# Kernel tuning notes

Hardware: AMD Instinct MI355X
Metric: run time of the kernel (lower is better)

Reference implementation:

```python
import jax, jax.numpy as jnp
import numpy as np

N = 50000
E = 1600000
D_IN = 128
D_OUT = 128


def setup_inputs() -> dict:
    key = jax.random.key(0)
    k1, k2, k3, k4, k5 = jax.random.split(key, 5)
    feature = jax.random.normal(k1, (N, D_IN), dtype=jnp.float32)
    src = jax.random.randint(k2, (E,), 0, N, dtype=jnp.int32)
    dst = jax.random.randint(k3, (E,), 0, N, dtype=jnp.int32)
    # nn.Linear(in_feats, out_feats): weight [out, in], bias [out]
    bound = 1.0 / np.sqrt(D_IN)
    weight = jax.random.uniform(k4, (D_OUT, D_IN), minval=-bound, maxval=bound, dtype=jnp.float32)
    bias = jax.random.uniform(k5, (D_OUT,), minval=-bound, maxval=bound, dtype=jnp.float32)
    return {"feature": feature, "src": src, "dst": dst, "weight": weight, "bias": bias}


def reference(feature, src, dst, weight, bias):
    # message: copy src node feature along each edge; reduce: mean over incoming edges
    msgs = feature[src]                              # [E, D_IN] irregular gather
    summed = jax.ops.segment_sum(msgs, dst, num_segments=N)          # [N, D_IN]
    deg = jax.ops.segment_sum(jnp.ones((E,), dtype=feature.dtype), dst, num_segments=N)  # [N]
    # DGL update_all: zero-in-degree nodes keep their original 'h' (feature)
    mean = summed / jnp.maximum(deg, 1.0)[:, None]
    h = jnp.where((deg > 0)[:, None], mean, feature)  # [N, D_IN]
    out = h @ weight.T + bias                          # Linear
    return jax.nn.relu(out)
```

## Files before the change

### kernel.cpp

```cpp
#include <hip/hip_runtime.h>


#define NN 50000
#define EE 1600000
#define DD 128
#define NSTRIP 3125
#define GSB 196
#define SCAP 12288
#define CH3 4096
#define NW3 391
#define NFB3 1563
#define WCAPQ 4096

typedef __attribute__((ext_vector_type(8))) short bf16x8;
typedef __attribute__((ext_vector_type(8))) unsigned short u16x8;
typedef __attribute__((ext_vector_type(4))) float f32x4;

static __device__ __forceinline__ short f2bf(float f) {
  union { float f; unsigned u; } x; x.f = f;
  unsigned r = (x.u + 0x7FFF + ((x.u >> 16) & 1)) >> 16;
  return (short)(r & 0xFFFF);
}

__global__ __launch_bounds__(1024) void k3(
    const int* __restrict__ src, const int* __restrict__ dst,
    int* __restrict__ gcur, unsigned int* __restrict__ ss,
    const float* __restrict__ feature, unsigned short* __restrict__ fb) {
  if (blockIdx.x < NW3) {
    __shared__ int cnt[GSB];
    __shared__ int curb[GSB];
    const int base = blockIdx.x * CH3;
    for (int i = threadIdx.x; i < GSB; i += 1024) cnt[i] = 0;
    __syncthreads();

    {
      int e0 = base + threadIdx.x * 4;
      if (e0 < EE) {
        int4 d4 = *(const int4*)(dst + e0);
        atomicAdd(&cnt[((unsigned)d4.x) >> 8], 1);
        atomicAdd(&cnt[((unsigned)d4.y) >> 8], 1);
        atomicAdd(&cnt[((unsigned)d4.z) >> 8], 1);
        atomicAdd(&cnt[((unsigned)d4.w) >> 8], 1);
      }
    }
    __syncthreads();

    for (int i = threadIdx.x; i < GSB; i += 1024) {
      int c = cnt[i];
      int b = (c > 0) ? atomicAdd(&gcur[i * 16], c) : 0;
      curb[i] = i * SCAP + b;
    }
    __syncthreads();

    {
      int e0 = base + threadIdx.x * 4;
      if (e0 < EE) {
        int4 s4 = *(const int4*)(src + e0);
        int4 d4 = *(const int4*)(dst + e0);
        {
          int p = atomicAdd(&curb[((unsigned)d4.x) >> 8], 1);
          ss[p] = (((unsigned)d4.x) << 16) | (unsigned)s4.x;
        }
        {
          int p = atomicAdd(&curb[((unsigned)d4.y) >> 8], 1);
          ss[p] = (((unsigned)d4.y) << 16) | (unsigned)s4.y;
        }
        {
          int p = atomicAdd(&curb[((unsigned)d4.z) >> 8], 1);
          ss[p] = (((unsigned)d4.z) << 16) | (unsigned)s4.z;
        }
        {
          int p = atomicAdd(&curb[((unsigned)d4.w) >> 8], 1);
          ss[p] = (((unsigned)d4.w) << 16) | (unsigned)s4.w;
        }
      }
    }
  } else {
    int i = (blockIdx.x - NW3) * 1024 + threadIdx.x;
    if (i < NN * DD / 4) {
      float4 v = ((const float4*)feature)[i];
      short4 o;
      o.x = f2bf(v.x); o.y = f2bf(v.y); o.z = f2bf(v.z); o.w = f2bf(v.w);
      ((short4*)fb)[i] = o;
    }
  }
}

__global__ __launch_bounds__(512) void fillagg(
    const unsigned int* __restrict__ ss, const int* __restrict__ gcur,
    const unsigned short* __restrict__ fb,
    unsigned short* __restrict__ hb) {
  __shared__ int win[WCAPQ];
  __shared__ int cur[256];
  __shared__ int rs[257];
  __shared__ int wsum2[4];
  const int g    = blockIdx.x >> 2;
  const int quar = blockIdx.x & 3;
  const int lo   = g * 256;
  const int nl_all = (NN - lo < 256) ? (NN - lo) : 256;
  int h0 = quar * 64;
  int h1 = h0 + 64;
  if (h1 > nl_all) h1 = nl_all;
  if (h1 < h0) h1 = h0;
  const int ebase = g * SCAP;
  const int eend  = ebase + gcur[g * 16];

  if (threadIdx.x < 256) cur[threadIdx.x] = 0;
  __syncthreads();
  for (int e = ebase + threadIdx.x; e < eend; e += 512) {
    atomicAdd(&cur[(ss[e] >> 16) & 255], 1);
  }
  __syncthreads();

  int x = 0;
  if (threadIdx.x < 256) {
    const int lane = threadIdx.x & 63;
    x = cur[threadIdx.x];
#pragma unroll
    for (int d = 1; d < 64; d <<= 1) { int t = __shfl_up(x, d, 64); if (lane >= d) x += t; }
    if (lane == 63) wsum2[threadIdx.x >> 6] = x;
  }
  __syncthreads();
  if (threadIdx.x < 256) {
    const int wv2 = threadIdx.x >> 6;
    int pre = 0;
#pragma unroll
    for (int k = 0; k < 4; ++k) pre += (k < wv2) ? wsum2[k] : 0;
    rs[threadIdx.x + 1] = pre + x;
    if (threadIdx.x == 0) rs[0] = 0;
    cur[threadIdx.x] = 0;
  }
  __syncthreads();

  const int wb = rs[h0];
  const int Th = rs[h1] - wb;
  const bool inlds = (Th <= WCAPQ);

  if (inlds) {
    for (int e = ebase + threadIdx.x; e < eend; e += 512) {
      unsigned pe = ss[e];
      int li = (pe >> 16) & 255;
      if (li >= h0 && li < h1) {
        int p = atomicAdd(&cur[li], 1);
        win[rs[li] - wb + p] = (int)(pe & 0xFFFFu);
      }
    }
  }
  __syncthreads();

  const int wv = threadIdx.x >> 6;
  const int lane = threadIdx.x & 63;
  const int q  = lane >> 4;
  const int sl = lane & 15;
  const u16x8* fp = (const u16x8*)fb;

  if (inlds) {
    for (int ln = h0 + wv; ln < h1; ln += 8) {
      const int st = rs[ln];
      const int en = rs[ln + 1];
      const int deg = en - st;
      const int n = lo + ln;

      float acc[8];
#pragma unroll
      for (int j = 0; j < 8; ++j) acc[j] = 0.f;

#pragma unroll 4
      for (int e = st + q; e < en; e += 4) {
        int s = win[e - wb];
        u16x8 v = fp[(size_t)s * 16 + sl];
#pragma unroll
        for (int j = 0; j < 8; ++j) {
          union { unsigned u; float f; } c; c.u = ((unsigned)v[j]) << 16;
          acc[j] += c.f;
        }
      }
#pragma unroll
      for (int j = 0; j < 8; ++j) {
        acc[j] += __shfl_xor(acc[j], 16, 64);
        acc[j] += __shfl_xor(acc[j], 32, 64);
      }

      if (q == 0) {
        u16x8 hv;
        if (deg > 0) {
          float inv = 1.0f / (float)deg;
#pragma unroll
          for (int j = 0; j < 8; ++j) hv[j] = (unsigned short)f2bf(acc[j] * inv);
        } else {
          hv = fp[(size_t)n * 16 + sl];
        }
        ((u16x8*)hb)[(size_t)n * 16 + sl] = hv;
      }
    }
  } else {
    for (int ln = h0 + wv; ln < h1; ln += 8) {
      const int deg = rs[ln + 1] - rs[ln];
      const int n = lo + ln;
      if (q == 0) {
        float acc[8];
#pragma unroll
        for (int j = 0; j < 8; ++j) acc[j] = 0.f;
        for (int e = ebase; e < eend; ++e) {
          unsigned pe = ss[e];
          if ((int)((pe >> 16) & 255) == ln) {
            u16x8 v = fp[(size_t)(pe & 0xFFFFu) * 16 + sl];
#pragma unroll
            for (int j = 0; j < 8; ++j) {
              union { unsigned u; float f; } c; c.u = ((unsigned)v[j]) << 16;
              acc[j] += c.f;
            }
          }
        }
        u16x8 hv;
        if (deg > 0) {
          float inv = 1.0f / (float)deg;
#pragma unroll
          for (int j = 0; j < 8; ++j) hv[j] = (unsigned short)f2bf(acc[j] * inv);
        } else {
          hv = fp[(size_t)n * 16 + sl];
        }
        ((u16x8*)hb)[(size_t)n * 16 + sl] = hv;
      }
    }
  }
}

__global__ __launch_bounds__(256) void mfma_gemm2(
    const short* __restrict__ hb,
    const float* __restrict__ weight,
    const float* __restrict__ bias,
    float* __restrict__ out) {
  __shared__ bf16x8 wfrag[2048];
  __shared__ float  bias_l[DD];

#pragma unroll
  for (int k = 0; k < 8; ++k) {
    int idx  = threadIdx.x * 8 + k;
    int ln   = idx & 63;
    int ct   = idx >> 6;
    int c    = ct >> 2;
    int t    = ct & 3;
    const float* wp = weight + (c * 16 + (ln & 15)) * DD + t * 32 + (ln >> 4) * 8;
    float4 w0 = *(const float4*)(wp);
    float4 w1 = *(const float4*)(wp + 4);
    bf16x8 b;
    b[0] = f2bf(w0.x); b[1] = f2bf(w0.y); b[2] = f2bf(w0.z); b[3] = f2bf(w0.w);
    b[4] = f2bf(w1.x); b[5] = f2bf(w1.y); b[6] = f2bf(w1.z); b[7] = f2bf(w1.w);
    wfrag[idx] = b;
  }
  if (threadIdx.x < DD) bias_l[threadIdx.x] = bias[threadIdx.x];
  __syncthreads();

  const int wave = threadIdx.x >> 6;
  const int lane = threadIdx.x & 63;
  const int r  = lane & 15;
  const int g  = lane >> 4;

#pragma unroll
  for (int s = 0; s < 2; ++s) {
    const int strip = blockIdx.x * 8 + wave * 2 + s;
    if (strip >= NSTRIP) continue;
    const int m0 = strip * 16;

    bf16x8 Af[4];
#pragma unroll
    for (int t = 0; t < 4; ++t) {
      Af[t] = *(const bf16x8*)(hb + (size_t)(m0 + r) * DD + t * 32 + g * 8);
    }

#pragma unroll
    for (int c = 0; c < 8; ++c) {
      f32x4 acc = {0.f, 0.f, 0.f, 0.f};
#pragma unroll
      for (int t = 0; t < 4; ++t) {
        acc = __builtin_amdgcn_mfma_f32_16x16x32_bf16(Af[t], wfrag[(c * 4 + t) * 64 + lane], acc, 0, 0, 0);
      }
      const float b = bias_l[c * 16 + r];
#pragma unroll
      for (int q = 0; q < 4; ++q) {
        int row = m0 + g * 4 + q;
        float v = acc[q] + b;
        out[(size_t)row * DD + c * 16 + r] = v > 0.f ? v : 0.f;
      }
    }
  }
}

extern "C" void kernel_launch(void* const* d_in, const int* in_sizes, int n_in,
                              void* d_out, int out_size, void* d_ws, size_t ws_size,
                              hipStream_t stream) {
  const float* feature = (const float*)d_in[0];
  const int*   src     = (const int*)d_in[1];
  const int*   dst     = (const int*)d_in[2];
  const float* weight  = (const float*)d_in[3];
  const float* bias    = (const float*)d_in[4];
  float* out = (float*)d_out;

  int* gcur = (int*)d_ws;
  unsigned short* hb = (unsigned short*)(gcur + 3136);

  unsigned int* ss = (unsigned int*)d_out;
  unsigned short* fb = (unsigned short*)((int*)d_out + GSB * SCAP);

  (void)hipMemsetAsync(gcur, 0, 3136 * sizeof(int), stream);

  k3<<<NW3 + NFB3, 1024, 0, stream>>>(src, dst, gcur, ss, feature, fb);
  fillagg<<<GSB * 4, 512, 0, stream>>>(ss, gcur, fb, hb);
  mfma_gemm2<<<(NSTRIP + 7) / 8, 256, 0, stream>>>((const short*)hb, weight, bias, out);
}
```

Measured before the change: 103.7 us.

## Shrink destination buckets to 64 nodes, one block per bucket

Edges are now bucketed into 64-node destination groups instead of 256-node groups. Each group is handled by a single 1024-thread block, replacing four 512-thread blocks that each scanned the whole 256-node bucket. This removes the four-fold redundant reads of the packed edge list and the serial fallback path for oversized windows. In exchange, the counter array in the binning kernel grows and there is no longer any overflow check. That relies on each 64-node bucket staying under 3072 edges.

```diff
diff --git a/kernel.cpp b/kernel.cpp
--- a/kernel.cpp
+++ b/kernel.cpp
@@ -5,12 +5,11 @@
 #define EE 1600000
 #define DD 128
 #define NSTRIP 3125
-#define GSB 196
-#define SCAP 12288
+#define GSB 782
+#define SCAP 3072
 #define CH3 4096
 #define NW3 391
 #define NFB3 1563
-#define WCAPQ 4096
 
 typedef __attribute__((ext_vector_type(8))) short bf16x8;
 typedef __attribute__((ext_vector_type(8))) unsigned short u16x8;
@@ -37,10 +36,10 @@
       int e0 = base + threadIdx.x * 4;
       if (e0 < EE) {
         int4 d4 = *(const int4*)(dst + e0);
-        atomicAdd(&cnt[((unsigned)d4.x) >> 8], 1);
-        atomicAdd(&cnt[((unsigned)d4.y) >> 8], 1);
-        atomicAdd(&cnt[((unsigned)d4.z) >> 8], 1);
-        atomicAdd(&cnt[((unsigned)d4.w) >> 8], 1);
+        atomicAdd(&cnt[((unsigned)d4.x) >> 6], 1);
+        atomicAdd(&cnt[((unsigned)d4.y) >> 6], 1);
+        atomicAdd(&cnt[((unsigned)d4.z) >> 6], 1);
+        atomicAdd(&cnt[((unsigned)d4.w) >> 6], 1);
       }
     }
     __syncthreads();
@@ -58,19 +57,19 @@
         int4 s4 = *(const int4*)(src + e0);
         int4 d4 = *(const int4*)(dst + e0);
         {
-          int p = atomicAdd(&curb[((unsigned)d4.x) >> 8], 1);
+          int p = atomicAdd(&curb[((unsigned)d4.x) >> 6], 1);
           ss[p] = (((unsigned)d4.x) << 16) | (unsigned)s4.x;
         }
         {
-          int p = atomicAdd(&curb[((unsigned)d4.y) >> 8], 1);
+          int p = atomicAdd(&curb[((unsigned)d4.y) >> 6], 1);
           ss[p] = (((unsigned)d4.y) << 16) | (unsigned)s4.y;
         }
         {
-          int p = atomicAdd(&curb[((unsigned)d4.z) >> 8], 1);
+          int p = atomicAdd(&curb[((unsigned)d4.z) >> 6], 1);
           ss[p] = (((unsigned)d4.z) << 16) | (unsigned)s4.z;
         }
         {
-          int p = atomicAdd(&curb[((unsigned)d4.w) >> 8], 1);
+          int p = atomicAdd(&curb[((unsigned)d4.w) >> 6], 1);
           ss[p] = (((unsigned)d4.w) << 16) | (unsigned)s4.w;
         }
       }
@@ -86,65 +85,43 @@
   }
 }
 
-__global__ __launch_bounds__(512) void fillagg(
+__global__ __launch_bounds__(1024) void fillagg(
     const unsigned int* __restrict__ ss, const int* __restrict__ gcur,
     const unsigned short* __restrict__ fb,
     unsigned short* __restrict__ hb) {
-  __shared__ int win[WCAPQ];
-  __shared__ int cur[256];
-  __shared__ int rs[257];
-  __shared__ int wsum2[4];
-  const int g    = blockIdx.x >> 2;
-  const int quar = blockIdx.x & 3;
-  const int lo   = g * 256;
-  const int nl_all = (NN - lo < 256) ? (NN - lo) : 256;
-  int h0 = quar * 64;
-  int h1 = h0 + 64;
-  if (h1 > nl_all) h1 = nl_all;
-  if (h1 < h0) h1 = h0;
+  __shared__ int win[SCAP];
+  __shared__ int cur[64];
+  __shared__ int rs[65];
+  const int g  = blockIdx.x;
+  const int lo = g * 64;
+  const int nl = (NN - lo < 64) ? (NN - lo) : 64;
   const int ebase = g * SCAP;
   const int eend  = ebase + gcur[g * 16];
 
-  if (threadIdx.x < 256) cur[threadIdx.x] = 0;
-  __syncthreads();
-  for (int e = ebase + threadIdx.x; e < eend; e += 512) {
-    atomicAdd(&cur[(ss[e] >> 16) & 255], 1);
-  }
-  __syncthreads();
-
-  int x = 0;
-  if (threadIdx.x < 256) {
-    const int lane = threadIdx.x & 63;
-    x = cur[threadIdx.x];
+  if (threadIdx.x < 64) cur[threadIdx.x] = 0;
+  __syncthreads();
+  for (int e = ebase + threadIdx.x; e < eend; e += 1024) {
+    atomicAdd(&cur[(ss[e] >> 16) & 63], 1);
+  }
+  __syncthreads();
+
+  if (threadIdx.x < 64) {
+    const int lane = threadIdx.x;
+    int v = cur[lane];
+    int x = v;
 #pragma unroll
     for (int d = 1; d < 64; d <<= 1) { int t = __shfl_up(x, d, 64); if (lane >= d) x += t; }
-    if (lane == 63) wsum2[threadIdx.x >> 6] = x;
-  }
-  __syncthreads();
-  if (threadIdx.x < 256) {
-    const int wv2 = threadIdx.x >> 6;
-    int pre = 0;
-#pragma unroll
-    for (int k = 0; k < 4; ++k) pre += (k < wv2) ? wsum2[k] : 0;
-    rs[threadIdx.x + 1] = pre + x;
-    if (threadIdx.x == 0) rs[0] = 0;
-    cur[threadIdx.x] = 0;
-  }
-  __syncthreads();
-
-  const int wb = rs[h0];
-  const int Th = rs[h1] - wb;
-  const bool inlds = (Th <= WCAPQ);
-
-  if (inlds) {
-    for (int e = ebase + threadIdx.x; e < eend; e += 512) {
-      unsigned pe = ss[e];
-      int li = (pe >> 16) & 255;
-      if (li >= h0 && li < h1) {
-        int p = atomicAdd(&cur[li], 1);
-        win[rs[li] - wb + p] = (int)(pe & 0xFFFFu);
-      }
-    }
+    rs[lane + 1] = x;
+    if (lane == 0) rs[0] = 0;
+    cur[lane] = 0;
+  }
+  __syncthreads();
+
+  for (int e = ebase + threadIdx.x; e < eend; e += 1024) {
+    unsigned pe = ss[e];
+    int li = (pe >> 16) & 63;
+    int p = atomicAdd(&cur[li], 1);
+    win[rs[li] + p] = (int)(pe & 0xFFFFu);
   }
   __syncthreads();
 
@@ -154,74 +131,42 @@
   const int sl = lane & 15;
   const u16x8* fp = (const u16x8*)fb;
 
-  if (inlds) {
-    for (int ln = h0 + wv; ln < h1; ln += 8) {
-      const int st = rs[ln];
-      const int en = rs[ln + 1];
-      const int deg = en - st;
-      const int n = lo + ln;
-
-      float acc[8];
-#pragma unroll
-      for (int j = 0; j < 8; ++j) acc[j] = 0.f;
+  for (int ln = wv; ln < nl; ln += 16) {
+    const int st = rs[ln];
+    const int en = rs[ln + 1];
+    const int deg = en - st;
+    const int n = lo + ln;
+
+    float acc[8];
+#pragma unroll
+    for (int j = 0; j < 8; ++j) acc[j] = 0.f;
 
 #pragma unroll 4
-      for (int e = st + q; e < en; e += 4) {
-        int s = win[e - wb];
-        u16x8 v = fp[(size_t)s * 16 + sl];
-#pragma unroll
-        for (int j = 0; j < 8; ++j) {
-          union { unsigned u; float f; } c; c.u = ((unsigned)v[j]) << 16;
-          acc[j] += c.f;
-        }
-      }
+    for (int e = st + q; e < en; e += 4) {
+      int s = win[e];
+      u16x8 v = fp[(size_t)s * 16 + sl];
 #pragma unroll
       for (int j = 0; j < 8; ++j) {
-        acc[j] += __shfl_xor(acc[j], 16, 64);
-        acc[j] += __shfl_xor(acc[j], 32, 64);
-      }
-
-      if (q == 0) {
-        u16x8 hv;
-        if (deg > 0) {
-          float inv = 1.0f / (float)deg;
-#pragma unroll
-          for (int j = 0; j < 8; ++j) hv[j] = (unsigned short)f2bf(acc[j] * inv);
-        } else {
-          hv = fp[(size_t)n * 16 + sl];
-        }
-        ((u16x8*)hb)[(size_t)n * 16 + sl] = hv;
-      }
-    }
-  } else {
-    for (int ln = h0 + wv; ln < h1; ln += 8) {
-      const int deg = rs[ln + 1] - rs[ln];
-      const int n = lo + ln;
-      if (q == 0) {
-        float acc[8];
-#pragma unroll
-        for (int j = 0; j < 8; ++j) acc[j] = 0.f;
-        for (int e = ebase; e < eend; ++e) {
-          unsigned pe = ss[e];
-          if ((int)((pe >> 16) & 255) == ln) {
-            u16x8 v = fp[(size_t)(pe & 0xFFFFu) * 16 + sl];
-#pragma unroll
-            for (int j = 0; j < 8; ++j) {
-              union { unsigned u; float f; } c; c.u = ((unsigned)v[j]) << 16;
-              acc[j] += c.f;
-            }
-          }
-        }
-        u16x8 hv;
-        if (deg > 0) {
-          float inv = 1.0f / (float)deg;
-#pragma unroll
-          for (int j = 0; j < 8; ++j) hv[j] = (unsigned short)f2bf(acc[j] * inv);
-        } else {
-          hv = fp[(size_t)n * 16 + sl];
-        }
-        ((u16x8*)hb)[(size_t)n * 16 + sl] = hv;
-      }
+        union { unsigned u; float f; } c; c.u = ((unsigned)v[j]) << 16;
+        acc[j] += c.f;
+      }
+    }
+#pragma unroll
+    for (int j = 0; j < 8; ++j) {
+      acc[j] += __shfl_xor(acc[j], 16, 64);
+      acc[j] += __shfl_xor(acc[j], 32, 64);
+    }
+
+    if (q == 0) {
+      u16x8 hv;
+      if (deg > 0) {
+        float inv = 1.0f / (float)deg;
+#pragma unroll
+        for (int j = 0; j < 8; ++j) hv[j] = (unsigned short)f2bf(acc[j] * inv);
+      } else {
+        hv = fp[(size_t)n * 16 + sl];
+      }
+      ((u16x8*)hb)[(size_t)n * 16 + sl] = hv;
     }
   }
 }
@@ -298,14 +243,14 @@
   float* out = (float*)d_out;
 
   int* gcur = (int*)d_ws;
-  unsigned short* hb = (unsigned short*)(gcur + 3136);
+  unsigned short* hb = (unsigned short*)(gcur + 12512);
 
   unsigned int* ss = (unsigned int*)d_out;
   unsigned short* fb = (unsigned short*)((int*)d_out + GSB * SCAP);
 
-  (void)hipMemsetAsync(gcur, 0, 3136 * sizeof(int), stream);
+  (void)hipMemsetAsync(gcur, 0, 12512 * sizeof(int), stream);
 
   k3<<<NW3 + NFB3, 1024, 0, stream>>>(src, dst, gcur, ss, feature, fb);
-  fillagg<<<GSB * 4, 512, 0, stream>>>(ss, gcur, fb, hb);
+  fillagg<<<GSB, 1024, 0, stream>>>(ss, gcur, fb, hb);
   mfma_gemm2<<<(NSTRIP + 7) / 8, 256, 0, stream>>>((const short*)hb, weight, bias, out);
 }
```

After: 105.3 us. Within noise of the previous version (+1.6%).
